# Performance work log

Hardware: AMD Instinct MI355X
Metric: run time of the kernel (lower is better)

## Reference

```python
import jax, jax.numpy as jnp
import numpy as np

B, S, DM, H = 2, 2048, 1024, 16
D = DM // H
SCALE = D ** -0.5


def setup_inputs() -> dict:
    key = jax.random.key(0)
    k1, k2, k3 = jax.random.split(key, 3)
    x = jax.random.normal(k1, (B, S, DM), dtype=jnp.float32)
    w_qkv = jax.random.normal(k2, (DM, 3 * DM), dtype=jnp.float32) * (DM ** -0.5)
    b_qkv = jnp.zeros((3 * DM,), dtype=jnp.float32)
    w_out = jax.random.normal(k3, (DM, DM), dtype=jnp.float32) * (DM ** -0.5)
    b_out = jnp.zeros((DM,), dtype=jnp.float32)
    return {"x": x, "w_qkv": w_qkv, "b_qkv": b_qkv, "w_out": w_out, "b_out": b_out}


def reference(x, w_qkv, b_qkv, w_out, b_out):
    b, n, _ = x.shape
    qkv = x @ w_qkv + b_qkv                          # [b, n, 3*dm]
    q, k, v = jnp.split(qkv, 3, axis=-1)
    # b n (h d) -> b h n d
    split = lambda t: t.reshape(b, n, H, D).transpose(0, 2, 1, 3)
    q, k, v = split(q), split(k), split(v)
    dots = jnp.einsum('bhid,bhjd->bhij', q, k) * SCALE
    # causal (fore) mask: -inf above the diagonal
    causal = jnp.tril(jnp.ones((n, n), dtype=bool))
    dots = jnp.where(causal, dots, -jnp.inf)
    attn = jax.nn.softmax(dots, axis=-1)
    out = jnp.einsum('bhij,bhjd->bhid', attn, v)     # [b, h, n, d]
    out = out.transpose(0, 2, 1, 3).reshape(b, n, H * D)
    return out @ w_out + b_out
```

## Files before the change

kernel.cpp:

```cpp
#include <hip/hip_runtime.h>
#include <hip/hip_bf16.h>

#define NB 2
#define NS 2048
#define NDM 1024
#define NH 16
#define ND 64
#define NM (NB * NS)
#define RS 3072
#define C1 0.1803368801111243f
#define THR_RAW 44.36141956f

typedef __attribute__((ext_vector_type(8))) short bf16x8;
typedef __attribute__((ext_vector_type(4))) float f32x4;

__device__ __forceinline__ unsigned short f2bf(float f) {
    unsigned int u = __float_as_uint(f);
    u += 0x7fffu + ((u >> 16) & 1u);
    return (unsigned short)(u >> 16);
}

__device__ __forceinline__ void gload16(const unsigned short* g, unsigned short* l) {
    __builtin_amdgcn_global_load_lds(
        (const __attribute__((address_space(1))) void*)g,
        (__attribute__((address_space(3))) void*)l, 16, 0, 0);
}

__global__ __launch_bounds__(256)
void convert_bf16(const float* __restrict__ in, unsigned short* __restrict__ out, int n8) {
    int i = blockIdx.x * 256 + threadIdx.x;
    const int stride = gridDim.x * 256;
    for (; i < n8; i += stride) {
        const float4 a = ((const float4*)in)[i * 2];
        const float4 b = ((const float4*)in)[i * 2 + 1];
        bf16x8 v;
        v[0] = (short)f2bf(a.x); v[1] = (short)f2bf(a.y);
        v[2] = (short)f2bf(a.z); v[3] = (short)f2bf(a.w);
        v[4] = (short)f2bf(b.x); v[5] = (short)f2bf(b.y);
        v[6] = (short)f2bf(b.z); v[7] = (short)f2bf(b.w);
        *(bf16x8*)(out + (size_t)i * 8) = v;
    }
}

__global__ __launch_bounds__(256)
void transpose_bf16(const float* __restrict__ W, unsigned short* __restrict__ WT,
                    int K, int N) {
    __shared__ float Ts[64][65];
    const int n0 = blockIdx.x * 64, k0 = blockIdx.y * 64;
    const int t = threadIdx.x;
    {
        const int c4 = (t & 15) * 4;
        #pragma unroll
        for (int p = 0; p < 4; p++) {
            const int r = (t >> 4) + p * 16;
            const float4 v = *(const float4*)(W + (size_t)(k0 + r) * N + n0 + c4);
            Ts[r][c4] = v.x; Ts[r][c4 + 1] = v.y; Ts[r][c4 + 2] = v.z; Ts[r][c4 + 3] = v.w;
        }
    }
    __syncthreads();
    {
        const int cc8 = (t & 7) * 8;
        #pragma unroll
        for (int p = 0; p < 2; p++) {
            const int rr = (t >> 3) + p * 32;
            bf16x8 v;
            #pragma unroll
            for (int j = 0; j < 8; j++) v[j] = (short)f2bf(Ts[cc8 + j][rr]);
            *(bf16x8*)(WT + (size_t)(n0 + rr) * K + k0 + cc8) = v;
        }
    }
}

__global__ __launch_bounds__(256)
void vtrans(const unsigned short* __restrict__ qkvb, unsigned short* __restrict__ vT) {
    __shared__ unsigned short Ts[64][65];
    const int st = blockIdx.x, bh = blockIdx.y;
    const int h = bh & (NH - 1), b = bh >> 4;
    const int t = threadIdx.x;
    {
        const int c8 = (t & 7) * 8;
        #pragma unroll
        for (int p = 0; p < 2; p++) {
            const int r = (t >> 3) + p * 32;
            const unsigned short* src =
                qkvb + (size_t)(b * NS + st * 64 + r) * RS + 2 * NDM + h * ND + c8;
            const bf16x8 v = *(const bf16x8*)src;
            #pragma unroll
            for (int j = 0; j < 8; j++) Ts[r][c8 + j] = (unsigned short)v[j];
        }
    }
    __syncthreads();
    {
        #pragma unroll
        for (int i = 0; i < 2; i++) {
            const int u = t + i * 256;
            const int d = u >> 3, cg = (u & 7) * 8;
            bf16x8 v;
            #pragma unroll
            for (int j = 0; j < 8; j++) v[j] = (short)Ts[cg + j][d];
            *(bf16x8*)(vT + ((size_t)bh * ND + d) * NS + st * 64 + cg) = v;
        }
    }
}

template<int MODE>
__global__ __launch_bounds__(256)
void gemm128(const unsigned short* __restrict__ A, const unsigned short* __restrict__ BT,
             const float* __restrict__ bias, void* __restrict__ Cv,
             int M, int N, int K) {
    __shared__ unsigned short As[128 * 32];
    __shared__ unsigned short Bs[128 * 32];

    const int t = threadIdx.x, lane = t & 63, wv = t >> 6;
    const int wm = wv >> 1, wn = wv & 1;
    const int m0 = blockIdx.y * 128, n0 = blockIdx.x * 128;
    const int fr = lane & 15, fg = lane >> 4;

    f32x4 acc[4][4];
    #pragma unroll
    for (int m = 0; m < 4; m++)
        #pragma unroll
        for (int n = 0; n < 4; n++)
            #pragma unroll
            for (int r = 0; r < 4; r++) acc[m][n][r] = 0.f;

    for (int k0 = 0; k0 < K; k0 += 32) {
        __syncthreads();
        #pragma unroll
        for (int i = 0; i < 2; i++) {
            const int u = t + i * 256;
            const int row = u >> 2;
            const int grp = (u & 3) ^ ((row ^ (row >> 2)) & 3);
            gload16(A  + (size_t)(m0 + row) * K + k0 + grp * 8, &As[(i * 256 + wv * 64) * 8]);
            gload16(BT + (size_t)(n0 + row) * K + k0 + grp * 8, &Bs[(i * 256 + wv * 64) * 8]);
        }
        __syncthreads();

        bf16x8 af[4], bfv[4];
        #pragma unroll
        for (int m = 0; m < 4; m++) {
            const int row = wm * 64 + m * 16 + fr;
            af[m] = *(const bf16x8*)&As[row * 32 + (fg ^ ((row ^ (row >> 2)) & 3)) * 8];
        }
        #pragma unroll
        for (int n = 0; n < 4; n++) {
            const int row = wn * 64 + n * 16 + fr;
            bfv[n] = *(const bf16x8*)&Bs[row * 32 + (fg ^ ((row ^ (row >> 2)) & 3)) * 8];
        }
        #pragma unroll
        for (int m = 0; m < 4; m++)
            #pragma unroll
            for (int n = 0; n < 4; n++)
                acc[m][n] = __builtin_amdgcn_mfma_f32_16x16x32_bf16(
                    af[m], bfv[n], acc[m][n], 0, 0, 0);
    }

    #pragma unroll
    for (int m = 0; m < 4; m++)
        #pragma unroll
        for (int n = 0; n < 4; n++) {
            const int col = n0 + wn * 64 + n * 16 + fr;
            const float bb = bias[col];
            #pragma unroll
            for (int rg = 0; rg < 4; rg++) {
                const int row = m0 + wm * 64 + m * 16 + fg * 4 + rg;
                const float v = acc[m][n][rg] + bb;
                if (MODE == 0) ((float*)Cv)[(size_t)row * N + col] = v;
                else ((unsigned short*)Cv)[(size_t)row * N + col] = f2bf(v);
            }
        }
}

__global__ __launch_bounds__(256)
void attn_mfma(const unsigned short* __restrict__ qkvb, const unsigned short* __restrict__ vT,
               unsigned short* __restrict__ atto) {
    const int bx = blockIdx.x;
    const int qt = (NS / 64 - 1) - (bx >> 5);
    const int bh = bx & 31;
    const int h = bh & (NH - 1), b = bh >> 4;
    const int q0 = qt * 64;
    const int t = threadIdx.x, lane = t & 63, wv = t >> 6;
    const int fr = lane & 15, fg = lane >> 4;

    __shared__ unsigned short Kt[2][64 * 64];
    __shared__ unsigned short Vt[2][64 * 64];
    __shared__ unsigned short Ps[4][16 * 64];

    const unsigned short* kb = qkvb + (size_t)b * NS * RS + NDM + h * ND;
    const unsigned short* vb = vT + (size_t)bh * ND * NS;

    bf16x8 qf[2];
    {
        const unsigned short* qrow =
            qkvb + (size_t)(b * NS + q0 + wv * 16 + fr) * RS + h * ND;
        qf[0] = *(const bf16x8*)(qrow + fg * 8);
        qf[1] = *(const bf16x8*)(qrow + 32 + fg * 8);
    }

    f32x4 oacc[4];
    #pragma unroll
    for (int d = 0; d < 4; d++)
        #pragma unroll
        for (int r = 0; r < 4; r++) oacc[d][r] = 0.f;
    float mrow[4] = {-INFINITY, -INFINITY, -INFINITY, -INFINITY};
    float nmC[4]  = {INFINITY, INFINITY, INFINITY, INFINITY};
    float lrow[4] = {0.f, 0.f, 0.f, 0.f};

    const int ntiles = qt + 1;

#define STAGE_KV(cbuf, jtile)                                                        \
    {                                                                                \
        _Pragma("unroll")                                                            \
        for (int i = 0; i < 2; i++) {                                                \
            const int u = t + i * 256;                                               \
            const int row = u >> 3;                                                  \
            const int grp = (u & 7) ^ (row & 7);                                     \
            gload16(kb + (size_t)((jtile) * 64 + row) * RS + grp * 8,                \
                    &Kt[cbuf][(i * 256 + wv * 64) * 8]);                             \
        }                                                                            \
        _Pragma("unroll")                                                            \
        for (int i = 0; i < 2; i++) {                                                \
            const int u = t + i * 256;                                               \
            const int row = u >> 3;                                                  \
            const int grp = (u & 7) ^ (row & 7);                                     \
            gload16(vb + (size_t)row * NS + (jtile) * 64 + grp * 8,                  \
                    &Vt[cbuf][(i * 256 + wv * 64) * 8]);                             \
        }                                                                            \
    }

    STAGE_KV(0, 0);

    for (int jt = 0; jt < ntiles; jt++) {
        const int cur = jt & 1;
        __syncthreads();
        if (jt + 1 < ntiles) STAGE_KV(cur ^ 1, jt + 1);

        f32x4 sacc[4];
        __builtin_amdgcn_s_setprio(1);
        #pragma unroll
        for (int kbi = 0; kbi < 4; kbi++) {
            #pragma unroll
            for (int r = 0; r < 4; r++) sacc[kbi][r] = 0.f;
            const int row = kbi * 16 + fr;
            const bf16x8 kf0 = *(const bf16x8*)&Kt[cur][row * 64 + ((fg) ^ (row & 7)) * 8];
            const bf16x8 kf1 = *(const bf16x8*)&Kt[cur][row * 64 + ((4 + fg) ^ (row & 7)) * 8];
            sacc[kbi] = __builtin_amdgcn_mfma_f32_16x16x32_bf16(qf[0], kf0, sacc[kbi], 0, 0, 0);
            sacc[kbi] = __builtin_amdgcn_mfma_f32_16x16x32_bf16(qf[1], kf1, sacc[kbi], 0, 0, 0);
        }
        __builtin_amdgcn_s_setprio(0);

        if (jt == ntiles - 1) {
            #pragma unroll
            for (int kbi = 0; kbi < 4; kbi++) {
                const int keyg = jt * 64 + kbi * 16 + fr;
                #pragma unroll
                for (int reg = 0; reg < 4; reg++) {
                    const int qg = q0 + wv * 16 + fg * 4 + reg;
                    if (keyg > qg) sacc[kbi][reg] = -INFINITY;
                }
            }
        }

        float pmax[4];
        #pragma unroll
        for (int reg = 0; reg < 4; reg++) {
            float pm = fmaxf(fmaxf(sacc[0][reg], sacc[1][reg]),
                             fmaxf(sacc[2][reg], sacc[3][reg]));
            pm = fmaxf(pm, __shfl_xor(pm, 1));
            pm = fmaxf(pm, __shfl_xor(pm, 2));
            pm = fmaxf(pm, __shfl_xor(pm, 4));
            pm = fmaxf(pm, __shfl_xor(pm, 8));
            pmax[reg] = pm;
        }
        bool need = false;
        #pragma unroll
        for (int reg = 0; reg < 4; reg++) need |= (pmax[reg] > mrow[reg] + THR_RAW);
        if (__any(need)) {
            #pragma unroll
            for (int reg = 0; reg < 4; reg++) {
                const float mn = fmaxf(mrow[reg], pmax[reg]);
                const float alpha = __builtin_amdgcn_exp2f((mrow[reg] - mn) * C1);
                mrow[reg] = mn;
                nmC[reg] = -mn * C1;
                lrow[reg] *= alpha;
                #pragma unroll
                for (int dblk = 0; dblk < 4; dblk++) oacc[dblk][reg] *= alpha;
            }
        }
        #pragma unroll
        for (int reg = 0; reg < 4; reg++) {
            float ps = 0.f;
            #pragma unroll
            for (int kbi = 0; kbi < 4; kbi++) {
                const float p = __builtin_amdgcn_exp2f(fmaf(sacc[kbi][reg], C1, nmC[reg]));
                sacc[kbi][reg] = p;
                ps += p;
            }
            ps += __shfl_xor(ps, 1);
            ps += __shfl_xor(ps, 2);
            ps += __shfl_xor(ps, 4);
            ps += __shfl_xor(ps, 8);
            lrow[reg] += ps;
        }

        #pragma unroll
        for (int kbi = 0; kbi < 4; kbi++) {
            const int colk = kbi * 16 + fr;
            #pragma unroll
            for (int reg = 0; reg < 4; reg++) {
                const int prow = fg * 4 + reg;
                Ps[wv][prow * 64 + (((colk >> 3) ^ (prow & 7)) << 3) + (colk & 7)] =
                    f2bf(sacc[kbi][reg]);
            }
        }

        bf16x8 pf[2];
        #pragma unroll
        for (int ks = 0; ks < 2; ks++)
            pf[ks] = *(const bf16x8*)&Ps[wv][fr * 64 + ((ks * 4 + fg) ^ (fr & 7)) * 8];
        __builtin_amdgcn_s_setprio(1);
        #pragma unroll
        for (int dblk = 0; dblk < 4; dblk++) {
            const int vrow = dblk * 16 + fr;
            #pragma unroll
            for (int ks = 0; ks < 2; ks++) {
                const bf16x8 vf =
                    *(const bf16x8*)&Vt[cur][vrow * 64 + ((ks * 4 + fg) ^ (vrow & 7)) * 8];
                oacc[dblk] = __builtin_amdgcn_mfma_f32_16x16x32_bf16(
                    pf[ks], vf, oacc[dblk], 0, 0, 0);
            }
        }
        __builtin_amdgcn_s_setprio(0);
    }
#undef STAGE_KV

    #pragma unroll
    for (int reg = 0; reg < 4; reg++) {
        const float inv = 1.f / lrow[reg];
        const int row = q0 + wv * 16 + fg * 4 + reg;
        unsigned short* dst = atto + ((size_t)b * NS + row) * NDM + h * ND;
        #pragma unroll
        for (int dblk = 0; dblk < 4; dblk++)
            dst[dblk * 16 + fr] = f2bf(oacc[dblk][reg] * inv);
    }
}

extern "C" void kernel_launch(void* const* d_in, const int* in_sizes, int n_in,
                              void* d_out, int out_size, void* d_ws, size_t ws_size,
                              hipStream_t stream) {
    const float* x     = (const float*)d_in[0];
    const float* w_qkv = (const float*)d_in[1];
    const float* b_qkv = (const float*)d_in[2];
    const float* w_out = (const float*)d_in[3];
    const float* b_out = (const float*)d_in[4];
    float* out = (float*)d_out;

    unsigned short* xb   = (unsigned short*)d_ws;
    unsigned short* wqT  = xb   + (size_t)NM * NDM;
    unsigned short* woT  = wqT  + (size_t)3 * NDM * NDM;
    unsigned short* qkvb = woT  + (size_t)NDM * NDM;
    unsigned short* vT   = qkvb + (size_t)NM * 3 * NDM;
    unsigned short* atto = xb;

    convert_bf16<<<2048, 256, 0, stream>>>(x, xb, NM * NDM / 8);
    transpose_bf16<<<dim3(3 * NDM / 64, NDM / 64), 256, 0, stream>>>(w_qkv, wqT, NDM, 3 * NDM);
    transpose_bf16<<<dim3(NDM / 64, NDM / 64), 256, 0, stream>>>(w_out, woT, NDM, NDM);

    gemm128<1><<<dim3(3 * NDM / 128, NM / 128), 256, 0, stream>>>(
        xb, wqT, b_qkv, qkvb, NM, 3 * NDM, NDM);

    vtrans<<<dim3(NS / 64, NB * NH), 256, 0, stream>>>(qkvb, vT);

    attn_mfma<<<dim3((NS / 64) * NB * NH), 256, 0, stream>>>(qkvb, vT, atto);

    gemm128<0><<<dim3(NDM / 128, NM / 128), 256, 0, stream>>>(
        atto, woT, b_out, out, NM, NDM, NDM);
}
```

Baseline: 215.5 us.

## Double-buffer GEMM LDS tiles and widen attention KV tiles to 128 keys

The GEMM kernel now double-buffers its A/B LDS tiles, prefetching the next 32-wide K slice while MFMAs run on the current one, and raises wave priority around the MFMA block. The attention kernel processes 128-key KV tiles instead of 64, halving loop iterations, barriers and online-softmax rescale checks per query tile. In exchange LDS use and register pressure rise, which may cut occupancy. Causal masking at 128 granularity also computes more fully masked keys on the last tile.

Measured after the change: 205.9 us. 4.4% less time.

```diff
diff --git a/kernel.cpp b/kernel.cpp
--- a/kernel.cpp
+++ b/kernel.cpp
@@ -108,8 +108,8 @@
 void gemm128(const unsigned short* __restrict__ A, const unsigned short* __restrict__ BT,
              const float* __restrict__ bias, void* __restrict__ Cv,
              int M, int N, int K) {
-    __shared__ unsigned short As[128 * 32];
-    __shared__ unsigned short Bs[128 * 32];
+    __shared__ unsigned short As[2][128 * 32];
+    __shared__ unsigned short Bs[2][128 * 32];
 
     const int t = threadIdx.x, lane = t & 63, wv = t >> 6;
     const int wm = wv >> 1, wn = wv & 1;
@@ -124,36 +124,56 @@
             #pragma unroll
             for (int r = 0; r < 4; r++) acc[m][n][r] = 0.f;
 
-    for (int k0 = 0; k0 < K; k0 += 32) {
+#define GSTAGE(buf, kk)                                                               \
+    {                                                                                 \
+        _Pragma("unroll")                                                             \
+        for (int i = 0; i < 2; i++) {                                                 \
+            const int u = t + i * 256;                                                \
+            const int row = u >> 2;                                                   \
+            const int grp = (u & 3) ^ ((row ^ (row >> 2)) & 3);                       \
+            gload16(A  + (size_t)(m0 + row) * K + (kk) + grp * 8,                     \
+                    &As[buf][(i * 256 + wv * 64) * 8]);                               \
+            gload16(BT + (size_t)(n0 + row) * K + (kk) + grp * 8,                     \
+                    &Bs[buf][(i * 256 + wv * 64) * 8]);                               \
+        }                                                                             \
+    }
+
+#define GCOMPUTE(buf)                                                                 \
+    {                                                                                 \
+        bf16x8 af[4], bfv[4];                                                         \
+        _Pragma("unroll")                                                             \
+        for (int m = 0; m < 4; m++) {                                                 \
+            const int row = wm * 64 + m * 16 + fr;                                    \
+            af[m] = *(const bf16x8*)&As[buf][row * 32 +                               \
+                        ((fg ^ ((row ^ (row >> 2)) & 3)) << 3)];                      \
+        }                                                                             \
+        _Pragma("unroll")                                                             \
+        for (int n = 0; n < 4; n++) {                                                 \
+            const int row = wn * 64 + n * 16 + fr;                                    \
+            bfv[n] = *(const bf16x8*)&Bs[buf][row * 32 +                              \
+                        ((fg ^ ((row ^ (row >> 2)) & 3)) << 3)];                      \
+        }                                                                             \
+        __builtin_amdgcn_s_setprio(1);                                                \
+        _Pragma("unroll")                                                             \
+        for (int m = 0; m < 4; m++)                                                   \
+            _Pragma("unroll")                                                         \
+            for (int n = 0; n < 4; n++)                                               \
+                acc[m][n] = __builtin_amdgcn_mfma_f32_16x16x32_bf16(                  \
+                    af[m], bfv[n], acc[m][n], 0, 0, 0);                               \
+        __builtin_amdgcn_s_setprio(0);                                                \
+    }
+
+    GSTAGE(0, 0);
+    for (int k0 = 0; k0 < K; k0 += 64) {
         __syncthreads();
-        #pragma unroll
-        for (int i = 0; i < 2; i++) {
-            const int u = t + i * 256;
-            const int row = u >> 2;
-            const int grp = (u & 3) ^ ((row ^ (row >> 2)) & 3);
-            gload16(A  + (size_t)(m0 + row) * K + k0 + grp * 8, &As[(i * 256 + wv * 64) * 8]);
-            gload16(BT + (size_t)(n0 + row) * K + k0 + grp * 8, &Bs[(i * 256 + wv * 64) * 8]);
-        }
+        GSTAGE(1, k0 + 32);
+        GCOMPUTE(0);
         __syncthreads();
-
-        bf16x8 af[4], bfv[4];
-        #pragma unroll
-        for (int m = 0; m < 4; m++) {
-            const int row = wm * 64 + m * 16 + fr;
-            af[m] = *(const bf16x8*)&As[row * 32 + (fg ^ ((row ^ (row >> 2)) & 3)) * 8];
-        }
-        #pragma unroll
-        for (int n = 0; n < 4; n++) {
-            const int row = wn * 64 + n * 16 + fr;
-            bfv[n] = *(const bf16x8*)&Bs[row * 32 + (fg ^ ((row ^ (row >> 2)) & 3)) * 8];
-        }
-        #pragma unroll
-        for (int m = 0; m < 4; m++)
-            #pragma unroll
-            for (int n = 0; n < 4; n++)
-                acc[m][n] = __builtin_amdgcn_mfma_f32_16x16x32_bf16(
-                    af[m], bfv[n], acc[m][n], 0, 0, 0);
-    }
+        if (k0 + 64 < K) GSTAGE(0, k0 + 64);
+        GCOMPUTE(1);
+    }
+#undef GSTAGE
+#undef GCOMPUTE
 
     #pragma unroll
     for (int m = 0; m < 4; m++)
@@ -182,9 +202,9 @@
     const int t = threadIdx.x, lane = t & 63, wv = t >> 6;
     const int fr = lane & 15, fg = lane >> 4;
 
-    __shared__ unsigned short Kt[2][64 * 64];
-    __shared__ unsigned short Vt[2][64 * 64];
-    __shared__ unsigned short Ps[4][16 * 64];
+    __shared__ unsigned short Kt[2][128 * 64];
+    __shared__ unsigned short Vt[2][64 * 128];
+    __shared__ unsigned short Ps[4][16 * 128];
 
     const unsigned short* kb = qkvb + (size_t)b * NS * RS + NDM + h * ND;
     const unsigned short* vb = vT + (size_t)bh * ND * NS;
@@ -206,24 +226,24 @@
     float nmC[4]  = {INFINITY, INFINITY, INFINITY, INFINITY};
     float lrow[4] = {0.f, 0.f, 0.f, 0.f};
 
-    const int ntiles = qt + 1;
+    const int ntiles = (qt >> 1) + 1;
 
 #define STAGE_KV(cbuf, jtile)                                                        \
     {                                                                                \
         _Pragma("unroll")                                                            \
-        for (int i = 0; i < 2; i++) {                                                \
+        for (int i = 0; i < 4; i++) {                                                \
             const int u = t + i * 256;                                               \
             const int row = u >> 3;                                                  \
             const int grp = (u & 7) ^ (row & 7);                                     \
-            gload16(kb + (size_t)((jtile) * 64 + row) * RS + grp * 8,                \
+            gload16(kb + (size_t)((jtile) * 128 + row) * RS + grp * 8,               \
                     &Kt[cbuf][(i * 256 + wv * 64) * 8]);                             \
         }                                                                            \
         _Pragma("unroll")                                                            \
-        for (int i = 0; i < 2; i++) {                                                \
+        for (int i = 0; i < 4; i++) {                                                \
             const int u = t + i * 256;                                               \
-            const int row = u >> 3;                                                  \
-            const int grp = (u & 7) ^ (row & 7);                                     \
-            gload16(vb + (size_t)row * NS + (jtile) * 64 + grp * 8,                  \
+            const int row = u >> 4;                                                  \
+            const int grp = (u & 15) ^ (row & 7);                                    \
+            gload16(vb + (size_t)row * NS + (jtile) * 128 + grp * 8,                 \
                     &Vt[cbuf][(i * 256 + wv * 64) * 8]);                             \
         }                                                                            \
     }
@@ -234,16 +254,18 @@
         const int cur = jt & 1;
         __syncthreads();
         if (jt + 1 < ntiles) STAGE_KV(cur ^ 1, jt + 1);
-
-        f32x4 sacc[4];
+        const unsigned short* Ktc = Kt[cur];
+        const unsigned short* Vtc = Vt[cur];
+
+        f32x4 sacc[8];
         __builtin_amdgcn_s_setprio(1);
         #pragma unroll
-        for (int kbi = 0; kbi < 4; kbi++) {
+        for (int kbi = 0; kbi < 8; kbi++) {
             #pragma unroll
             for (int r = 0; r < 4; r++) sacc[kbi][r] = 0.f;
             const int row = kbi * 16 + fr;
-            const bf16x8 kf0 = *(const bf16x8*)&Kt[cur][row * 64 + ((fg) ^ (row & 7)) * 8];
-            const bf16x8 kf1 = *(const bf16x8*)&Kt[cur][row * 64 + ((4 + fg) ^ (row & 7)) * 8];
+            const bf16x8 kf0 = *(const bf16x8*)&Ktc[row * 64 + (((fg) ^ (row & 7)) << 3)];
+            const bf16x8 kf1 = *(const bf16x8*)&Ktc[row * 64 + (((4 + fg) ^ (row & 7)) << 3)];
             sacc[kbi] = __builtin_amdgcn_mfma_f32_16x16x32_bf16(qf[0], kf0, sacc[kbi], 0, 0, 0);
             sacc[kbi] = __builtin_amdgcn_mfma_f32_16x16x32_bf16(qf[1], kf1, sacc[kbi], 0, 0, 0);
         }
@@ -251,8 +273,8 @@
 
         if (jt == ntiles - 1) {
             #pragma unroll
-            for (int kbi = 0; kbi < 4; kbi++) {
-                const int keyg = jt * 64 + kbi * 16 + fr;
+            for (int kbi = 0; kbi < 8; kbi++) {
+                const int keyg = jt * 128 + kbi * 16 + fr;
                 #pragma unroll
                 for (int reg = 0; reg < 4; reg++) {
                     const int qg = q0 + wv * 16 + fg * 4 + reg;
@@ -264,8 +286,10 @@
         float pmax[4];
         #pragma unroll
         for (int reg = 0; reg < 4; reg++) {
-            float pm = fmaxf(fmaxf(sacc[0][reg], sacc[1][reg]),
-                             fmaxf(sacc[2][reg], sacc[3][reg]));
+            float pm = fmaxf(fmaxf(fmaxf(sacc[0][reg], sacc[1][reg]),
+                                   fmaxf(sacc[2][reg], sacc[3][reg])),
+                             fmaxf(fmaxf(sacc[4][reg], sacc[5][reg]),
+                                   fmaxf(sacc[6][reg], sacc[7][reg])));
             pm = fmaxf(pm, __shfl_xor(pm, 1));
             pm = fmaxf(pm, __shfl_xor(pm, 2));
             pm = fmaxf(pm, __shfl_xor(pm, 4));
@@ -291,7 +315,7 @@
         for (int reg = 0; reg < 4; reg++) {
             float ps = 0.f;
             #pragma unroll
-            for (int kbi = 0; kbi < 4; kbi++) {
+            for (int kbi = 0; kbi < 8; kbi++) {
                 const float p = __builtin_amdgcn_exp2f(fmaf(sacc[kbi][reg], C1, nmC[reg]));
                 sacc[kbi][reg] = p;
                 ps += p;
@@ -304,28 +328,28 @@
         }
 
         #pragma unroll
-        for (int kbi = 0; kbi < 4; kbi++) {
+        for (int kbi = 0; kbi < 8; kbi++) {
             const int colk = kbi * 16 + fr;
             #pragma unroll
             for (int reg = 0; reg < 4; reg++) {
                 const int prow = fg * 4 + reg;
-                Ps[wv][prow * 64 + (((colk >> 3) ^ (prow & 7)) << 3) + (colk & 7)] =
+                Ps[wv][prow * 128 + (((colk >> 3) ^ (prow & 7)) << 3) + (colk & 7)] =
                     f2bf(sacc[kbi][reg]);
             }
         }
 
-        bf16x8 pf[2];
-        #pragma unroll
-        for (int ks = 0; ks < 2; ks++)
-            pf[ks] = *(const bf16x8*)&Ps[wv][fr * 64 + ((ks * 4 + fg) ^ (fr & 7)) * 8];
+        bf16x8 pf[4];
+        #pragma unroll
+        for (int ks = 0; ks < 4; ks++)
+            pf[ks] = *(const bf16x8*)&Ps[wv][fr * 128 + (((ks * 4 + fg) ^ (fr & 7)) << 3)];
         __builtin_amdgcn_s_setprio(1);
         #pragma unroll
         for (int dblk = 0; dblk < 4; dblk++) {
             const int vrow = dblk * 16 + fr;
             #pragma unroll
-            for (int ks = 0; ks < 2; ks++) {
+            for (int ks = 0; ks < 4; ks++) {
                 const bf16x8 vf =
-                    *(const bf16x8*)&Vt[cur][vrow * 64 + ((ks * 4 + fg) ^ (vrow & 7)) * 8];
+                    *(const bf16x8*)&Vtc[vrow * 128 + (((ks * 4 + fg) ^ (vrow & 7)) << 3)];
                 oacc[dblk] = __builtin_amdgcn_mfma_f32_16x16x32_bf16(
                     pf[ks], vf, oacc[dblk], 0, 0, 0);
             }
```
